# Kernel tuning notes

Measured on AMD Instinct MI355X. Metric: run time of the kernel, lower is better.

Reference implementation:

```python
import jax, jax.numpy as jnp
import numpy as np
import math

D_MODEL = 1024
HEADS = 16
D_K = D_MODEL // HEADS
D_FF = 2048
EPS = 1e-6
NEG = -1e9


def _layernorm(x, gamma, beta):
    mu = x.mean(axis=-1, keepdims=True)
    var = ((x - mu) ** 2).mean(axis=-1, keepdims=True)
    return gamma * (x - mu) / jnp.sqrt(var + EPS) + beta


def setup_inputs() -> dict:
    key = jax.random.key(0)
    ks = jax.random.split(key, 12)
    B, S = 8, 1024
    s = 0.02
    return {
        "x": jax.random.normal(ks[0], (B, S, D_MODEL), jnp.float32),
        "mask": jnp.ones((B, 1, S), jnp.int32),
        "wq": jax.random.normal(ks[1], (D_MODEL, D_MODEL), jnp.float32) * s,
        "bq": jnp.zeros((D_MODEL,), jnp.float32),
        "wk": jax.random.normal(ks[2], (D_MODEL, D_MODEL), jnp.float32) * s,
        "bk": jnp.zeros((D_MODEL,), jnp.float32),
        "wv": jax.random.normal(ks[3], (D_MODEL, D_MODEL), jnp.float32) * s,
        "bv": jnp.zeros((D_MODEL,), jnp.float32),
        "wo": jax.random.normal(ks[4], (D_MODEL, D_MODEL), jnp.float32) * s,
        "bo": jnp.zeros((D_MODEL,), jnp.float32),
        "w1": jax.random.normal(ks[5], (D_MODEL, D_FF), jnp.float32) * s,
        "b1": jnp.zeros((D_FF,), jnp.float32),
        "w2": jax.random.normal(ks[6], (D_FF, D_MODEL), jnp.float32) * s,
        "b2": jnp.zeros((D_MODEL,), jnp.float32),
        "g1": jnp.ones((D_MODEL,), jnp.float32),
        "be1": jnp.zeros((D_MODEL,), jnp.float32),
        "g2": jnp.ones((D_MODEL,), jnp.float32),
        "be2": jnp.zeros((D_MODEL,), jnp.float32),
    }


def reference(x, mask, wq, bq, wk, bk, wv, bv, wo, bo, w1, b1, w2, b2, g1, be1, g2, be2):
    B, S, _ = x.shape
    # QKV projections, split heads: [B,H,S,d_k]
    q = (x @ wq + bq).reshape(B, S, HEADS, D_K).transpose(0, 2, 1, 3)
    k = (x @ wk + bk).reshape(B, S, HEADS, D_K).transpose(0, 2, 1, 3)
    v = (x @ wv + bv).reshape(B, S, HEADS, D_K).transpose(0, 2, 1, 3)
    scores = jnp.einsum("bhqd,bhkd->bhqk", q, k) / math.sqrt(D_K)
    m = mask[:, None, :, :]  # [B,1,1|S,S] broadcast over heads
    scores = jnp.where(m == 0, NEG, scores)
    attn = jax.nn.softmax(scores, axis=-1)
    out = jnp.einsum("bhqk,bhkd->bhqd", attn, v)
    concat = out.transpose(0, 2, 1, 3).reshape(B, S, D_MODEL)
    attn_out = concat @ wo + bo
    x1 = _layernorm(x + attn_out, g1, be1)
    ff = jax.nn.relu(x1 @ w1 + b1) @ w2 + b2
    return _layernorm(x1 + ff, g2, be2)
```

## Files before the change

### kernel.cpp

```cpp
#include <hip/hip_runtime.h>
#include <stdint.h>

using u16 = unsigned short;
using u32 = unsigned int;
typedef __attribute__((ext_vector_type(4))) float f32x4;
typedef __attribute__((ext_vector_type(8))) short s16x8;

#define LOG2E 1.44269504088896340736f
#define SCL (0.125f * LOG2E)

__device__ __forceinline__ u16 f2b(float f) {
  union { float f; u32 u; } v; v.f = f;
  u32 r = v.u + 0x7fffu + ((v.u >> 16) & 1u);
  return (u16)(r >> 16);
}

__device__ __forceinline__ float b2f(u16 x) {
  union { u32 u; float f; } v; v.u = (u32)x << 16; return v.f;
}

__device__ __forceinline__ u32 pack2(u16 lo, u16 hi) {
  return (u32)lo | ((u32)hi << 16);
}

__device__ __forceinline__ u32 cvtpk(float lo, float hi) {
  u32 r;
  asm("v_cvt_pk_bf16_f32 %0, %1, %2" : "=v"(r) : "v"(lo), "v"(hi));
  return r;
}

__device__ __forceinline__ float fexp2(float x) {
  float t = fmaf(x, 8388608.f, 1065053744.f);
  t = fmaxf(t, 0.f);
  union { u32 u; float f; } v; v.u = (u32)t;
  return v.f;
}

__device__ __forceinline__ f32x4 mfma16(s16x8 a, s16x8 b, f32x4 c) {
  return __builtin_amdgcn_mfma_f32_16x16x32_bf16(a, b, c, 0, 0, 0);
}

__device__ __forceinline__ void gload16(const void* g, void* l) {
  __builtin_amdgcn_global_load_lds(
      (const __attribute__((address_space(1))) void*)g,
      (__attribute__((address_space(3))) void*)l, 16, 0, 0);
}

__global__ __launch_bounds__(256) void cvt_bf16(const float* __restrict__ in,
                                                u16* __restrict__ out, int n4) {
  int i = blockIdx.x * 256 + threadIdx.x;
  if (i >= n4) return;
  float4 v = ((const float4*)in)[i];
  uint2 o;
  o.x = pack2(f2b(v.x), f2b(v.y));
  o.y = pack2(f2b(v.z), f2b(v.w));
  ((uint2*)out)[i] = o;
}

__device__ __forceinline__ void tr_tile(const float* __restrict__ in,
                                        u16* __restrict__ outT,
                                        int K, int N, int bx, int by,
                                        float (*t)[33]) {
  int n0 = bx * 32, k0 = by * 32;
  int tx = threadIdx.x, ty = threadIdx.y;
#pragma unroll
  for (int i = 0; i < 4; i++)
    t[ty + i * 8][tx] = in[(size_t)(k0 + ty + i * 8) * N + n0 + tx];
  __syncthreads();
#pragma unroll
  for (int i = 0; i < 4; i++)
    outT[(size_t)(n0 + ty + i * 8) * K + k0 + tx] = f2b(t[tx][ty + i * 8]);
}

__global__ __launch_bounds__(256) void prep(const float* __restrict__ wq,
                                            const float* __restrict__ wk,
                                            const float* __restrict__ wv,
                                            const float* __restrict__ wo,
                                            const float* __restrict__ w1,
                                            const float* __restrict__ w2,
                                            const float* __restrict__ bq,
                                            const float* __restrict__ bk,
                                            u16* __restrict__ wqt,
                                            u16* __restrict__ wkt,
                                            u16* __restrict__ wvt,
                                            u16* __restrict__ wot,
                                            u16* __restrict__ w1t,
                                            u16* __restrict__ w2t,
                                            float* __restrict__ bqk) {
  __shared__ float t[32][33];
  int id = blockIdx.x;
  if (id < 4096) {
    int seg = id >> 10, lid = id & 1023;
    const float* in = seg == 0 ? wq : seg == 1 ? wk : seg == 2 ? wv : wo;
    u16* out = seg == 0 ? wqt : seg == 1 ? wkt : seg == 2 ? wvt : wot;
    tr_tile(in, out, 1024, 1024, lid & 31, lid >> 5, t);
  } else if (id < 6144) {
    int lid = id - 4096;
    tr_tile(w1, w1t, 1024, 2048, lid & 63, lid >> 6, t);
  } else if (id < 8192) {
    int lid = id - 6144;
    tr_tile(w2, w2t, 2048, 1024, lid & 31, lid >> 5, t);
  } else {
    int i = (id - 8192) * 256 + threadIdx.y * 32 + threadIdx.x;
    bqk[i] = (i < 1024) ? bq[i] : bk[i - 1024];
  }
}

template <int EPI>
__global__ __launch_bounds__(512, 1) void gemmhk(const u16* __restrict__ A,
                                                 const u16* __restrict__ Bt,
                                                 const float* __restrict__ bias,
                                                 void* __restrict__ outp,
                                                 int N, int K) {
  __shared__ u16 As[2][2][128 * 64];
  __shared__ u16 Bs[2][2][128 * 64];
  int tid = threadIdx.x;
  int wv = tid >> 6, ln = tid & 63;
  int fr = ln & 15, fg = ln >> 4;
  int wm = wv >> 2, wn = wv & 3;

  int x = blockIdx.x & 7;
  int l = blockIdx.x >> 3;
  int m0 = (x * 4 + (l & 3)) * 256;
  int n0 = (l >> 2) * 256;

  const u16* Abase = A + (size_t)m0 * K;
  const u16* Bbase = Bt + (size_t)n0 * K;

  auto stageAq = [&](int buf, int h, int r0, int kt) {
    int row = tid >> 3, ch = tid & 7;
    int csw = ch ^ ((r0 + row) & 7);
    gload16(Abase + (size_t)(h * 128 + r0 + row) * K + kt * 64 + csw * 8,
            &As[buf][h][(size_t)(r0 * 8 + (wv << 6)) * 8]);
  };
  auto stageBh = [&](int buf, int h, int kt) {
#pragma unroll
    for (int s = 0; s < 2; s++) {
      int idx = s * 512 + tid;
      int row = idx >> 3, ch = idx & 7;
      int csw = ch ^ (row & 7);
      gload16(Bbase + (size_t)(h * 128 + row) * K + kt * 64 + csw * 8,
              &Bs[buf][h][(size_t)(s * 512 + (wv << 6)) * 8]);
    }
  };

  f32x4 acc[8][4] = {};
  int NT = K >> 6;

  stageAq(0, 0, 0, 0); stageAq(0, 1, 0, 0); stageBh(0, 0, 0);
  stageAq(0, 0, 64, 0); stageAq(0, 1, 64, 0); stageBh(0, 1, 0);

  for (int t = 0; t < NT; ++t) {
    int buf = t & 1, nbuf = buf ^ 1;
    int tn = (t + 1 < NT) ? t + 1 : t;
    const u16* Ah = &As[buf][wm][0];
    const u16* B0p = &Bs[buf][0][0];
    const u16* B1p = &Bs[buf][1][0];
    s16x8 a[4][2], b0[2][2], b1[2][2];

    asm volatile("s_waitcnt vmcnt(4)" ::: "memory");
    __builtin_amdgcn_s_barrier();
    __builtin_amdgcn_sched_barrier(0);
#pragma unroll
    for (int q = 0; q < 4; q++) {
      int row = q * 16 + fr;
#pragma unroll
      for (int ks = 0; ks < 2; ks++)
        a[q][ks] = *(const s16x8*)(Ah + row * 64 + (((ks * 4 + fg) ^ (row & 7)) << 3));
    }
#pragma unroll
    for (int pj = 0; pj < 2; pj++) {
      int row = wn * 32 + pj * 16 + fr;
#pragma unroll
      for (int ks = 0; ks < 2; ks++)
        b0[pj][ks] = *(const s16x8*)(B0p + row * 64 + (((ks * 4 + fg) ^ (row & 7)) << 3));
    }
    stageAq(nbuf, 0, 0, tn); stageAq(nbuf, 1, 0, tn); stageBh(nbuf, 0, tn);
    __builtin_amdgcn_sched_barrier(0);
    __builtin_amdgcn_s_setprio(1);
#pragma unroll
    for (int q = 0; q < 4; q++)
#pragma unroll
      for (int pj = 0; pj < 2; pj++) {
        acc[q][pj] = mfma16(a[q][0], b0[pj][0], acc[q][pj]);
        acc[q][pj] = mfma16(a[q][1], b0[pj][1], acc[q][pj]);
      }
    __builtin_amdgcn_s_setprio(0);
    __builtin_amdgcn_sched_barrier(0);

    asm volatile("s_waitcnt vmcnt(4)" ::: "memory");
    __builtin_amdgcn_s_barrier();
    __builtin_amdgcn_sched_barrier(0);
#pragma unroll
    for (int pj = 0; pj < 2; pj++) {
      int row = wn * 32 + pj * 16 + fr;
#pragma unroll
      for (int ks = 0; ks < 2; ks++)
        b1[pj][ks] = *(const s16x8*)(B1p + row * 64 + (((ks * 4 + fg) ^ (row & 7)) << 3));
    }
    stageAq(nbuf, 0, 64, tn); stageAq(nbuf, 1, 64, tn); stageBh(nbuf, 1, tn);
    __builtin_amdgcn_sched_barrier(0);
    __builtin_amdgcn_s_setprio(1);
#pragma unroll
    for (int q = 0; q < 4; q++)
#pragma unroll
      for (int pj = 0; pj < 2; pj++) {
        acc[q][2 + pj] = mfma16(a[q][0], b1[pj][0], acc[q][2 + pj]);
        acc[q][2 + pj] = mfma16(a[q][1], b1[pj][1], acc[q][2 + pj]);
      }
    __builtin_amdgcn_s_setprio(0);
    __builtin_amdgcn_sched_barrier(0);

#pragma unroll
    for (int q = 0; q < 4; q++) {
      int row = 64 + q * 16 + fr;
#pragma unroll
      for (int ks = 0; ks < 2; ks++)
        a[q][ks] = *(const s16x8*)(Ah + row * 64 + (((ks * 4 + fg) ^ (row & 7)) << 3));
    }
    __builtin_amdgcn_sched_barrier(0);
    __builtin_amdgcn_s_setprio(1);
#pragma unroll
    for (int q = 0; q < 4; q++)
#pragma unroll
      for (int pj = 0; pj < 2; pj++) {
        acc[4 + q][2 + pj] = mfma16(a[q][0], b1[pj][0], acc[4 + q][2 + pj]);
        acc[4 + q][2 + pj] = mfma16(a[q][1], b1[pj][1], acc[4 + q][2 + pj]);
      }
    __builtin_amdgcn_s_setprio(0);

    __builtin_amdgcn_s_setprio(1);
#pragma unroll
    for (int q = 0; q < 4; q++)
#pragma unroll
      for (int pj = 0; pj < 2; pj++) {
        acc[4 + q][pj] = mfma16(a[q][0], b0[pj][0], acc[4 + q][pj]);
        acc[4 + q][pj] = mfma16(a[q][1], b0[pj][1], acc[4 + q][pj]);
      }
    __builtin_amdgcn_s_setprio(0);
    __builtin_amdgcn_sched_barrier(0);
  }

#pragma unroll
  for (int j = 0; j < 4; j++) {
    int coll = n0 + (j >> 1) * 128 + wn * 32 + (j & 1) * 16 + fr;
    float bv = bias[coll];
#pragma unroll
    for (int i = 0; i < 8; i++) {
      int rowbase = m0 + wm * 128 + (i >> 2) * 64 + (i & 3) * 16 + fg * 4;
      if (EPI == 5) {
        u16* o = (u16*)outp + (size_t)(coll >> 10) * (8192u * 1024u) + (coll & 1023);
#pragma unroll
        for (int r = 0; r < 4; r++)
          o[(size_t)(rowbase + r) * 1024] = f2b(acc[i][j][r] + bv);
      } else {
#pragma unroll
        for (int r = 0; r < 4; r++) {
          float v = acc[i][j][r] + bv;
          if (EPI == 2) v = v > 0.f ? v : 0.f;
          ((u16*)outp)[(size_t)(rowbase + r) * N + coll] = f2b(v);
        }
      }
    }
  }
}

template <int EPI, int BN, int WM, int WN>
__global__ __launch_bounds__(512, 1) void gemm8(const u16* __restrict__ A,
                                                const u16* __restrict__ Bt,
                                                const float* __restrict__ bias,
                                                void* __restrict__ outp,
                                                int N, int K) {
  constexpr int MI = 256 / (WM * 16);
  constexpr int NJ = BN / (WN * 16);
  constexpr int BB = BN / 128;
  __shared__ u16 As[4][256 * 32];
  __shared__ u16 Bs[4][BN * 32];
  int tid = threadIdx.x;
  int wv = tid >> 6, ln = tid & 63;
  int fr = ln & 15, fg = ln >> 4;
  int wm = wv / WN, wn = wv % WN;

  int x = blockIdx.x & 7;
  int l = blockIdx.x >> 3;
  int m0 = (x * 4 + (l & 3)) * 256;
  int n0 = (l >> 2) * BN;

  auto stageA = [&](int buf, int kt) {
#pragma unroll
    for (int s = 0; s < 2; s++) {
      int idx = s * 512 + tid;
      int row = idx >> 2, ch = idx & 3;
      int sw = (row ^ (row >> 2)) & 3;
      int gcol = kt * 32 + ((ch ^ sw) << 3);
      gload16(A + (size_t)(m0 + row) * K + gcol,
              &As[buf][(size_t)(s * 512 + (wv << 6)) * 8]);
    }
  };
  auto stageB = [&](int buf, int kt) {
#pragma unroll
    for (int s = 0; s < BB; s++) {
      int idx = s * 512 + tid;
      int row = idx >> 2, ch = idx & 3;
      int sw = (row ^ (row >> 2)) & 3;
      int gcol = kt * 32 + ((ch ^ sw) << 3);
      gload16(Bt + (size_t)(n0 + row) * K + gcol,
              &Bs[buf][(size_t)(s * 512 + (wv << 6)) * 8]);
    }
  };

  f32x4 acc[MI][NJ] = {};
  int NT = K >> 5;

#pragma unroll
  for (int tt = 0; tt < 3; ++tt) { stageA(tt, tt); stageB(tt, tt); }

  for (int t = 0; t < NT; ++t) {
    if constexpr (BN == 256) asm volatile("s_waitcnt vmcnt(8)" ::: "memory");
    else                     asm volatile("s_waitcnt vmcnt(6)" ::: "memory");
    __builtin_amdgcn_s_barrier();
    __builtin_amdgcn_sched_barrier(0);

    const u16* Ab = As[t & 3];
    const u16* Bb = Bs[t & 3];
    s16x8 af[MI], bf[NJ];
#pragma unroll
    for (int j = 0; j < NJ; j++) {
      int row = wn * (BN / WN) + j * 16 + fr;
      int sw = (row ^ (row >> 2)) & 3;
      bf[j] = *(const s16x8*)&Bb[row * 32 + ((fg ^ sw) << 3)];
    }
#pragma unroll
    for (int i = 0; i < MI; i++) {
      int row = wm * (256 / WM) + i * 16 + fr;
      int sw = (row ^ (row >> 2)) & 3;
      af[i] = *(const s16x8*)&Ab[row * 32 + ((fg ^ sw) << 3)];
    }

    int tn = (t + 3 < NT) ? t + 3 : NT - 1;
    stageA((t + 3) & 3, tn);
    stageB((t + 3) & 3, tn);

    __builtin_amdgcn_sched_barrier(0);
    __builtin_amdgcn_s_setprio(1);
#pragma unroll
    for (int i = 0; i < MI; i++)
#pragma unroll
      for (int j = 0; j < NJ; j++)
        acc[i][j] = mfma16(af[i], bf[j], acc[i][j]);
    __builtin_amdgcn_s_setprio(0);
    __builtin_amdgcn_sched_barrier(0);
  }

#pragma unroll
  for (int j = 0; j < NJ; j++) {
    int coll = n0 + wn * (BN / WN) + j * 16 + fr;
    float bv = bias[coll];
#pragma unroll
    for (int i = 0; i < MI; i++) {
      int rowbase = m0 + wm * (256 / WM) + i * 16 + fg * 4;
      if (EPI == 3) {
        int b_ = rowbase >> 10, s_ = rowbase & 1023;
        int h_ = coll >> 6, d_ = coll & 63;
        float v0 = acc[i][j][0] + bv, v1 = acc[i][j][1] + bv;
        float v2 = acc[i][j][2] + bv, v3 = acc[i][j][3] + bv;
        uint2 o; o.x = pack2(f2b(v0), f2b(v1)); o.y = pack2(f2b(v2), f2b(v3));
        *(uint2*)((u16*)outp + (((size_t)((b_ * 16 + h_) * 64 + d_)) << 10) + s_) = o;
      } else {
#pragma unroll
        for (int r = 0; r < 4; r++) {
          int row = rowbase + r;
          float v = acc[i][j][r] + bv;
          ((u16*)outp)[(size_t)row * N + coll] = f2b(v);
        }
      }
    }
  }
}

__global__ __launch_bounds__(256) void attn_fwd(const u16* __restrict__ q,
                                                const u16* __restrict__ k,
                                                const u16* __restrict__ vT,
                                                const int* __restrict__ mask,
                                                u16* __restrict__ ctx) {
  __shared__ u16 Ks[64 * 64];
  __shared__ u16 Vs[2][64 * 64];
  __shared__ u16 Ps[4][32 * 64];
  int tid = threadIdx.x, wv = tid >> 6, ln = tid & 63;
  int fr = ln & 15, fg = ln >> 4;
  int bh = blockIdx.x, b = bh >> 4, h = bh & 15;
  int q0 = blockIdx.y * 128;

  const u16* kbase = k + (size_t)b * 1024 * 1024 + h * 64;
  const u16* vbase = vT + (size_t)bh * 64 * 1024;

  int cl0 = wv * 64 + ln, cl1 = cl0 + 256;
  int rr0 = cl0 >> 3, csw0 = (cl0 & 7) ^ (rr0 & 7);
  int rr1 = cl1 >> 3, csw1 = (cl1 & 7) ^ (rr1 & 7);
  const u16* kc0 = kbase + rr0 * 1024 + csw0 * 8;
  const u16* kc1 = kbase + rr1 * 1024 + csw1 * 8;
  const u16* vc0 = vbase + rr0 * 1024 + csw0 * 8;
  const u16* vc1 = vbase + rr1 * 1024 + csw1 * 8;
  u16* Kd0 = Ks + (size_t)(wv * 64) * 8;
  u16* Kd1 = Kd0 + 256 * 8;

  gload16(kc0, Kd0); gload16(kc1, Kd1);
  gload16(vc0, Vs[0] + (size_t)(wv * 64) * 8);
  gload16(vc1, Vs[0] + (size_t)(wv * 64 + 256) * 8);
  kc0 += 65536; kc1 += 65536; vc0 += 64; vc1 += 64;

  int okm = 1;
#pragma unroll
  for (int t4 = 0; t4 < 4; t4++) {
    int4 mv = ((const int4*)(mask + b * 1024))[ln * 4 + t4];
    okm &= (mv.x != 0) & (mv.y != 0) & (mv.z != 0) & (mv.w != 0);
  }
  int seq_ok = __all(okm);

  s16x8 qf[2][2];
#pragma unroll
  for (int i = 0; i < 2; i++)
#pragma unroll
    for (int ks = 0; ks < 2; ks++) {
      int row = q0 + wv * 32 + i * 16 + fr;
      qf[i][ks] = *(const s16x8*)(q + (size_t)(b * 1024 + row) * 1024 + h * 64 + ks * 32 + fg * 8);
      u32* qw = (u32*)&qf[i][ks];
#pragma unroll
      for (int w = 0; w < 4; w++) {
        union { u32 u; float f; } lo, hi;
        lo.u = qw[w] << 16; hi.u = qw[w] & 0xffff0000u;
        qw[w] = cvtpk(lo.f * SCL, hi.f * SCL);
      }
    }

  s16x8 ones;
#pragma unroll
  for (int j = 0; j < 8; j++) ones[j] = (short)0x3F80;

  f32x4 ao[2][4] = {};
  f32x4 aol[2] = {};
  u16* Pw = Ps[wv];

  __syncthreads();

  for (int kt = 0; kt < 16; ++kt) {
    int cur = kt & 1;

    f32x4 st[4][2] = {};
    __builtin_amdgcn_s_setprio(1);
#pragma unroll
    for (int ks = 0; ks < 2; ks++)
#pragma unroll
      for (int jm = 0; jm < 4; jm++) {
        s16x8 kfr = *(const s16x8*)(Ks + (jm * 16 + fr) * 64 + (((ks * 4 + fg) ^ (fr & 7)) << 3));
        st[jm][0] = mfma16(kfr, qf[0][ks], st[jm][0]);
        st[jm][1] = mfma16(kfr, qf[1][ks], st[jm][1]);
      }
    __builtin_amdgcn_s_setprio(0);

    __syncthreads();
    if (kt < 15) {
      u16* Vd = Vs[cur ^ 1];
      gload16(kc0, Kd0); gload16(kc1, Kd1);
      gload16(vc0, Vd + (size_t)(wv * 64) * 8);
      gload16(vc1, Vd + (size_t)(wv * 64 + 256) * 8);
      kc0 += 65536; kc1 += 65536; vc0 += 64; vc1 += 64;
    }

    if (!seq_ok) {
#pragma unroll
      for (int jm = 0; jm < 4; jm++) {
        int4 mv = *(const int4*)(mask + b * 1024 + kt * 64 + jm * 16 + fg * 4);
        float m0 = mv.x == 0 ? -1e9f * SCL : 0.f;
        float m1 = mv.y == 0 ? -1e9f * SCL : 0.f;
        float m2 = mv.z == 0 ? -1e9f * SCL : 0.f;
        float m3 = mv.w == 0 ? -1e9f * SCL : 0.f;
#pragma unroll
        for (int i = 0; i < 2; i++) {
          st[jm][i][0] += m0; st[jm][i][1] += m1;
          st[jm][i][2] += m2; st[jm][i][3] += m3;
        }
      }
    }

#pragma unroll
    for (int i = 0; i < 2; i++)
#pragma unroll
      for (int jm = 0; jm < 4; jm++)
#pragma unroll
        for (int r = 0; r < 4; r++)
          st[jm][i][r] = fexp2(st[jm][i][r]);

#pragma unroll
    for (int i = 0; i < 2; i++) {
      int qrow = i * 16 + fr;
      int rowoff = qrow * 64;
      int sw = (qrow & 7) << 3;
#pragma unroll
      for (int jm = 0; jm < 4; jm++) {
        uint2 pk;
        pk.x = cvtpk(st[jm][i][0], st[jm][i][1]);
        pk.y = cvtpk(st[jm][i][2], st[jm][i][3]);
        *(uint2*)(Pw + ((rowoff + jm * 16 + fg * 4) ^ sw)) = pk;
      }
    }

    const u16* Vc = Vs[cur];
    __builtin_amdgcn_s_setprio(1);
#pragma unroll
    for (int ks = 0; ks < 2; ks++) {
      int ch = ((ks * 4 + fg) ^ (fr & 7)) << 3;
      s16x8 pa0 = *(const s16x8*)(Pw + fr * 64 + ch);
      s16x8 pa1 = *(const s16x8*)(Pw + (16 + fr) * 64 + ch);
#pragma unroll
      for (int jd = 0; jd < 4; jd++) {
        s16x8 bv = *(const s16x8*)(Vc + (jd * 16 + fr) * 64 + ch);
        ao[0][jd] = mfma16(pa0, bv, ao[0][jd]);
        ao[1][jd] = mfma16(pa1, bv, ao[1][jd]);
      }
      aol[0] = mfma16(pa0, ones, aol[0]);
      aol[1] = mfma16(pa1, ones, aol[1]);
    }
    __builtin_amdgcn_s_setprio(0);

    __syncthreads();
  }

#pragma unroll
  for (int io = 0; io < 2; io++) {
    float i0 = 1.f / aol[io][0], i1 = 1.f / aol[io][1];
    float i2 = 1.f / aol[io][2], i3 = 1.f / aol[io][3];
#pragma unroll
    for (int jd = 0; jd < 4; jd++) {
      int d = jd * 16 + fr;
      int rowb = wv * 32 + io * 16 + fg * 4;
      u16* cb = ctx + (size_t)(b * 1024 + q0 + rowb) * 1024 + h * 64 + d;
      cb[0]    = f2b(ao[io][jd][0] * i0);
      cb[1024] = f2b(ao[io][jd][1] * i1);
      cb[2048] = f2b(ao[io][jd][2] * i2);
      cb[3072] = f2b(ao[io][jd][3] * i3);
    }
  }
}

template <bool ABF16, bool BBF16>
__global__ __launch_bounds__(256) void ln_fused(const void* __restrict__ a,
                                                const void* __restrict__ bsrc,
                                                const float* __restrict__ gamma,
                                                const float* __restrict__ beta,
                                                float* __restrict__ outf,
                                                u16* __restrict__ outb) {
  int row = blockIdx.x, tid = threadIdx.x;
  float v0, v1, v2, v3;
  if (ABF16) {
    uint2 va = ((const uint2*)((const u16*)a + (size_t)row * 1024))[tid];
    v0 = b2f((u16)(va.x & 0xffff)); v1 = b2f((u16)(va.x >> 16));
    v2 = b2f((u16)(va.y & 0xffff)); v3 = b2f((u16)(va.y >> 16));
  } else {
    float4 va = ((const float4*)((const float*)a + (size_t)row * 1024))[tid];
    v0 = va.x; v1 = va.y; v2 = va.z; v3 = va.w;
  }
  if (BBF16) {
    uint2 vb = ((const uint2*)((const u16*)bsrc + (size_t)row * 1024))[tid];
    v0 += b2f((u16)(vb.x & 0xffff)); v1 += b2f((u16)(vb.x >> 16));
    v2 += b2f((u16)(vb.y & 0xffff)); v3 += b2f((u16)(vb.y >> 16));
  } else {
    float4 vb = ((const float4*)((const float*)bsrc + (size_t)row * 1024))[tid];
    v0 += vb.x; v1 += vb.y; v2 += vb.z; v3 += vb.w;
  }
  float s = v0 + v1 + v2 + v3;
  float ss = v0 * v0 + v1 * v1 + v2 * v2 + v3 * v3;
#pragma unroll
  for (int m = 1; m < 64; m <<= 1) { s += __shfl_xor(s, m); ss += __shfl_xor(ss, m); }
  __shared__ float rs[8];
  int wv = tid >> 6;
  if ((tid & 63) == 0) { rs[wv] = s; rs[4 + wv] = ss; }
  __syncthreads();
  s = rs[0] + rs[1] + rs[2] + rs[3];
  ss = rs[4] + rs[5] + rs[6] + rs[7];
  float mu = s * (1.f / 1024.f);
  float var = ss * (1.f / 1024.f) - mu * mu;
  float rstd = rsqrtf(var + 1e-6f);
  float4 g4 = ((const float4*)gamma)[tid];
  float4 be4 = ((const float4*)beta)[tid];
  float y0 = g4.x * (v0 - mu) * rstd + be4.x;
  float y1 = g4.y * (v1 - mu) * rstd + be4.y;
  float y2 = g4.z * (v2 - mu) * rstd + be4.z;
  float y3 = g4.w * (v3 - mu) * rstd + be4.w;
  if (outf) {
    float4 o; o.x = y0; o.y = y1; o.z = y2; o.w = y3;
    ((float4*)(outf + (size_t)row * 1024))[tid] = o;
  }
  if (outb) {
    uint2 ob; ob.x = pack2(f2b(y0), f2b(y1)); ob.y = pack2(f2b(y2), f2b(y3));
    ((uint2*)(outb + (size_t)row * 1024))[tid] = ob;
  }
}

extern "C" void kernel_launch(void* const* d_in, const int* in_sizes, int n_in,
                              void* d_out, int out_size, void* d_ws, size_t ws_size,
                              hipStream_t stream) {
  const float* x   = (const float*)d_in[0];
  const int*   msk = (const int*)d_in[1];
  const float* wq  = (const float*)d_in[2];
  const float* bq  = (const float*)d_in[3];
  const float* wk  = (const float*)d_in[4];
  const float* bk  = (const float*)d_in[5];
  const float* wv  = (const float*)d_in[6];
  const float* bv  = (const float*)d_in[7];
  const float* wo  = (const float*)d_in[8];
  const float* bo  = (const float*)d_in[9];
  const float* w1  = (const float*)d_in[10];
  const float* b1  = (const float*)d_in[11];
  const float* w2  = (const float*)d_in[12];
  const float* b2  = (const float*)d_in[13];
  const float* g1  = (const float*)d_in[14];
  const float* be1 = (const float*)d_in[15];
  const float* g2  = (const float*)d_in[16];
  const float* be2 = (const float*)d_in[17];
  float* out = (float*)d_out;
  char* ws = (char*)d_ws;
  const size_t MB = 1u << 20;

  u16* xb  = (u16*)(ws + 0);
  u16* wqt = (u16*)(ws + 16 * MB);
  u16* wkt = (u16*)(ws + 18 * MB);
  u16* wvt = (u16*)(ws + 20 * MB);
  u16* wot = (u16*)(ws + 22 * MB);
  u16* w1t = (u16*)(ws + 24 * MB);
  u16* w2t = (u16*)(ws + 28 * MB);
  u16* qb  = (u16*)(ws + 32 * MB);
  u16* kb  = (u16*)(ws + 48 * MB);
  u16* vT  = (u16*)(ws + 64 * MB);
  u16* ctx = (u16*)(ws + 80 * MB);
  float* bqk = (float*)(ws + 80 * MB);
  u16* attn_out = (u16*)(ws + 32 * MB);
  u16* x1b = (u16*)(ws + 0);
  u16* hb  = (u16*)(ws + 96 * MB);
  u16* fff = (u16*)(ws + 48 * MB);

  cvt_bf16<<<8192, 256, 0, stream>>>(x, xb, 8192 * 1024 / 4);
  prep<<<8200, dim3(32, 8), 0, stream>>>(wq, wk, wv, wo, w1, w2, bq, bk,
                                         wqt, wkt, wvt, wot, w1t, w2t, bqk);

  gemmhk<5><<<256, 512, 0, stream>>>(xb, wqt, bqk, qb, 2048, 1024);
  gemm8<3, 128, 4, 2><<<256, 512, 0, stream>>>(xb, wvt, bv, vT, 1024, 1024);

  attn_fwd<<<dim3(128, 8), 256, 0, stream>>>(qb, kb, vT, msk, ctx);

  gemm8<0, 128, 4, 2><<<256, 512, 0, stream>>>(ctx, wot, bo, attn_out, 1024, 1024);
  ln_fused<true, true><<<8192, 256, 0, stream>>>(xb, attn_out, g1, be1, nullptr, x1b);
  gemmhk<2><<<256, 512, 0, stream>>>(x1b, w1t, b1, hb, 2048, 1024);
  gemm8<0, 128, 4, 2><<<256, 512, 0, stream>>>(hb, w2t, b2, fff, 1024, 2048);
  ln_fused<true, true><<<8192, 256, 0, stream>>>(x1b, fff, g2, be2, out, nullptr);
}
```

Baseline: 250.8 us.

## Deepen GEMM global-to-LDS prefetch to two tiles ahead

Restructures the double-buffered GEMM main loop so global loads are issued two K-tiles ahead instead of one. Each LDS buffer is refilled in place as soon as its fragments have been read into registers. The staging helpers are unified into one generic `stage` routine, and the wait becomes a single vmcnt(8) per iteration. This gives global memory more time to hide latency, at the cost of four workgroup barriers per iteration instead of two, plus some redundant reloads on the final tiles.

```diff
diff --git a/kernel.cpp b/kernel.cpp
--- a/kernel.cpp
+++ b/kernel.cpp
@@ -127,38 +127,38 @@
   const u16* Abase = A + (size_t)m0 * K;
   const u16* Bbase = Bt + (size_t)n0 * K;
 
-  auto stageAq = [&](int buf, int h, int r0, int kt) {
-    int row = tid >> 3, ch = tid & 7;
-    int csw = ch ^ ((r0 + row) & 7);
-    gload16(Abase + (size_t)(h * 128 + r0 + row) * K + kt * 64 + csw * 8,
-            &As[buf][h][(size_t)(r0 * 8 + (wv << 6)) * 8]);
-  };
-  auto stageBh = [&](int buf, int h, int kt) {
-#pragma unroll
-    for (int s = 0; s < 2; s++) {
-      int idx = s * 512 + tid;
+  auto stage = [&](const u16* gbase, u16* lbase, int kt) {
+#pragma unroll
+    for (int rnd = 0; rnd < 2; rnd++) {
+      int idx = rnd * 512 + tid;
       int row = idx >> 3, ch = idx & 7;
       int csw = ch ^ (row & 7);
-      gload16(Bbase + (size_t)(h * 128 + row) * K + kt * 64 + csw * 8,
-              &Bs[buf][h][(size_t)(s * 512 + (wv << 6)) * 8]);
+      gload16(gbase + (size_t)row * K + kt * 64 + csw * 8,
+              lbase + (size_t)(rnd * 512 + (wv << 6)) * 8);
     }
   };
 
   f32x4 acc[8][4] = {};
   int NT = K >> 6;
 
-  stageAq(0, 0, 0, 0); stageAq(0, 1, 0, 0); stageBh(0, 0, 0);
-  stageAq(0, 0, 64, 0); stageAq(0, 1, 64, 0); stageBh(0, 1, 0);
+  stage(Bbase,                   &Bs[0][0][0], 0);
+  stage(Bbase + (size_t)128 * K, &Bs[0][1][0], 0);
+  stage(Abase,                   &As[0][0][0], 0);
+  stage(Abase + (size_t)128 * K, &As[0][1][0], 0);
+  stage(Bbase,                   &Bs[1][0][0], 1);
+  stage(Bbase + (size_t)128 * K, &Bs[1][1][0], 1);
+  stage(Abase,                   &As[1][0][0], 1);
+  stage(Abase + (size_t)128 * K, &As[1][1][0], 1);
 
   for (int t = 0; t < NT; ++t) {
-    int buf = t & 1, nbuf = buf ^ 1;
-    int tn = (t + 1 < NT) ? t + 1 : t;
+    int buf = t & 1;
+    int tn2 = (t + 2 < NT) ? t + 2 : NT - 1;
     const u16* Ah = &As[buf][wm][0];
     const u16* B0p = &Bs[buf][0][0];
     const u16* B1p = &Bs[buf][1][0];
     s16x8 a[4][2], b0[2][2], b1[2][2];
 
-    asm volatile("s_waitcnt vmcnt(4)" ::: "memory");
+    asm volatile("s_waitcnt vmcnt(8)" ::: "memory");
     __builtin_amdgcn_s_barrier();
     __builtin_amdgcn_sched_barrier(0);
 #pragma unroll
@@ -175,8 +175,6 @@
       for (int ks = 0; ks < 2; ks++)
         b0[pj][ks] = *(const s16x8*)(B0p + row * 64 + (((ks * 4 + fg) ^ (row & 7)) << 3));
     }
-    stageAq(nbuf, 0, 0, tn); stageAq(nbuf, 1, 0, tn); stageBh(nbuf, 0, tn);
-    __builtin_amdgcn_sched_barrier(0);
     __builtin_amdgcn_s_setprio(1);
 #pragma unroll
     for (int q = 0; q < 4; q++)
@@ -188,9 +186,9 @@
     __builtin_amdgcn_s_setprio(0);
     __builtin_amdgcn_sched_barrier(0);
 
-    asm volatile("s_waitcnt vmcnt(4)" ::: "memory");
     __builtin_amdgcn_s_barrier();
     __builtin_amdgcn_sched_barrier(0);
+    stage(Bbase, &Bs[buf][0][0], tn2);
 #pragma unroll
     for (int pj = 0; pj < 2; pj++) {
       int row = wn * 32 + pj * 16 + fr;
@@ -198,8 +196,6 @@
       for (int ks = 0; ks < 2; ks++)
         b1[pj][ks] = *(const s16x8*)(B1p + row * 64 + (((ks * 4 + fg) ^ (row & 7)) << 3));
     }
-    stageAq(nbuf, 0, 64, tn); stageAq(nbuf, 1, 64, tn); stageBh(nbuf, 1, tn);
-    __builtin_amdgcn_sched_barrier(0);
     __builtin_amdgcn_s_setprio(1);
 #pragma unroll
     for (int q = 0; q < 4; q++)
@@ -211,6 +207,9 @@
     __builtin_amdgcn_s_setprio(0);
     __builtin_amdgcn_sched_barrier(0);
 
+    __builtin_amdgcn_s_barrier();
+    __builtin_amdgcn_sched_barrier(0);
+    stage(Bbase + (size_t)128 * K, &Bs[buf][1][0], tn2);
 #pragma unroll
     for (int q = 0; q < 4; q++) {
       int row = 64 + q * 16 + fr;
@@ -218,7 +217,6 @@
       for (int ks = 0; ks < 2; ks++)
         a[q][ks] = *(const s16x8*)(Ah + row * 64 + (((ks * 4 + fg) ^ (row & 7)) << 3));
     }
-    __builtin_amdgcn_sched_barrier(0);
     __builtin_amdgcn_s_setprio(1);
 #pragma unroll
     for (int q = 0; q < 4; q++)
@@ -228,7 +226,12 @@
         acc[4 + q][2 + pj] = mfma16(a[q][1], b1[pj][1], acc[4 + q][2 + pj]);
       }
     __builtin_amdgcn_s_setprio(0);
-
+    __builtin_amdgcn_sched_barrier(0);
+
+    __builtin_amdgcn_s_barrier();
+    __builtin_amdgcn_sched_barrier(0);
+    stage(Abase,                   &As[buf][0][0], tn2);
+    stage(Abase + (size_t)128 * K, &As[buf][1][0], tn2);
     __builtin_amdgcn_s_setprio(1);
 #pragma unroll
     for (int q = 0; q < 4; q++)
```

After: 261.2 us. 1.04x slower.
